# Kernel optimization log

Hardware: AMD Instinct MI355X
Metric: run time of the kernel (lower is better)

The kernel has to match this reference:

```python
import jax, jax.numpy as jnp
import numpy as np

MIN_TIMESCALE = 1.0
MAX_TIMESCALE = 10000.0


def llama_rope(x):
    # x: [B, S, N, H]; LLaMA-style interleaved rotary embedding (pairs along last dim).
    B, S, N, H = x.shape
    half = H // 2
    fraction = 2.0 * jnp.arange(0, half, dtype=jnp.float32) / H
    timescale = MIN_TIMESCALE * (MAX_TIMESCALE / MIN_TIMESCALE) ** fraction  # [half]
    position = jnp.arange(S, dtype=jnp.float32)[None, :, None, None]  # [1,S,1,1]
    sinusoid = position / timescale[None, None, None, :]  # [1,S,1,half]
    sin, cos = jnp.sin(sinusoid), jnp.cos(sinusoid)
    xr = x.astype(jnp.float32).reshape(B, S, N, half, 2)
    x1, x2 = xr[..., 0], xr[..., 1]
    r1 = x1 * cos - x2 * sin
    r2 = x2 * cos + x1 * sin
    out = jnp.stack((r1, r2), axis=-1).reshape(B, S, N, H)
    return out.astype(x.dtype)


def setup_inputs() -> dict:
    key = jax.random.key(0)
    kx, kq, kk, kv, ko = jax.random.split(key, 5)
    B, S, D, N, H = 4, 2048, 2048, 16, 128
    x = jax.random.normal(kx, (B, S, D), dtype=jnp.float32)
    # fan_in-style scaling for projection kernels
    wq = jax.random.normal(kq, (D, N, H), dtype=jnp.float32) / np.sqrt(D)
    wk = jax.random.normal(kk, (D, N, H), dtype=jnp.float32) / np.sqrt(D)
    wv = jax.random.normal(kv, (D, N, H), dtype=jnp.float32) / np.sqrt(D)
    wo = jax.random.normal(ko, (N, H, D), dtype=jnp.float32) / np.sqrt(N * H)
    return {"x": x, "wq": wq, "wk": wk, "wv": wv, "wo": wo}


def reference(x, wq, wk, wv, wo):
    # QKV projections (DenseGeneral with features=(num_heads, head_dim))
    q = jnp.einsum("bsd,dnh->bsnh", x, wq)
    k = jnp.einsum("bsd,dnh->bsnh", x, wk)
    v = jnp.einsum("bsd,dnh->bsnh", x, wv)
    # Fused RoPE on query and key (LLaMA interleaved variant)
    q = llama_rope(q)
    k = llama_rope(k)
    head_dim = q.shape[-1]
    q = q / jnp.sqrt(jnp.asarray(head_dim, q.dtype))
    # Causal flash attention (math equivalent: masked softmax attention)
    S = q.shape[1]
    logits = jnp.einsum("bqnh,bknh->bnqk", q, k)  # [B,N,S,S]
    causal = jnp.tril(jnp.ones((S, S), dtype=bool))
    logits = jnp.where(causal[None, None, :, :], logits, jnp.asarray(-1e30, logits.dtype))
    probs = jax.nn.softmax(logits.astype(jnp.float32), axis=-1).astype(v.dtype)
    attn = jnp.einsum("bnqk,bknh->bqnh", probs, v)  # [B,S,N,H]
    # Output projection (DenseGeneral over axes (-2,-1))
    return jnp.einsum("bqnh,nhd->bqd", attn, wo)
```

## Files before the change

kernel.cpp:

```cpp
#include <hip/hip_runtime.h>
#include <hip/hip_bf16.h>
#include <cmath>

#define S_LEN 2048
#define DDIM  2048
#define NHEAD 16
#define HDIM  128
#define BATCH 4
#define KPAD  152
#define VPAD  40
#define PPAD  40

typedef __bf16 bf16;
typedef __attribute__((ext_vector_type(8))) __bf16 bf16x8;
typedef __attribute__((ext_vector_type(4))) __bf16 bf16x4;
typedef __attribute__((ext_vector_type(4))) float  f32x4;

__device__ __forceinline__ void gl_lds(const bf16* g, bf16* l) {
  __builtin_amdgcn_global_load_lds((const __attribute__((address_space(1))) unsigned*)g,
                                   (__attribute__((address_space(3))) unsigned*)l, 16, 0, 0);
}

__global__ __launch_bounds__(256)
void conv_kernel(const float* __restrict__ x, bf16* __restrict__ y) {
  size_t i = ((size_t)blockIdx.x * 256 + threadIdx.x) * 8;
  float4 a = *(const float4*)&x[i];
  float4 b = *(const float4*)&x[i + 4];
  bf16x8 o;
  o[0] = (bf16)a.x; o[1] = (bf16)a.y; o[2] = (bf16)a.z; o[3] = (bf16)a.w;
  o[4] = (bf16)b.x; o[5] = (bf16)b.y; o[6] = (bf16)b.z; o[7] = (bf16)b.w;
  *(bf16x8*)&y[i] = o;
}

__global__ __launch_bounds__(256)
void twconv_kernel(const float* __restrict__ W, bf16* __restrict__ Wt) {
  __shared__ bf16 tile[64][72];
  const int t  = threadIdx.x;
  const int k0 = blockIdx.x * 64;
  const int n0 = blockIdx.y * 64;
#pragma unroll
  for (int it = 0; it < 4; it++) {
    int k = (t >> 4) + it * 16;
    int n = (t & 15) * 4;
    float4 v = *(const float4*)&W[(size_t)(k0 + k) * DDIM + n0 + n];
    tile[k][n + 0] = (bf16)v.x; tile[k][n + 1] = (bf16)v.y;
    tile[k][n + 2] = (bf16)v.z; tile[k][n + 3] = (bf16)v.w;
  }
  __syncthreads();
#pragma unroll
  for (int it = 0; it < 2; it++) {
    int n  = (t >> 3) + it * 32;
    int kc = (t & 7) * 8;
    bf16x8 o;
#pragma unroll
    for (int j = 0; j < 8; j++) o[j] = tile[kc + j][n];
    *(bf16x8*)&Wt[(size_t)(n0 + n) * DDIM + k0 + kc] = o;
  }
}

template <int MODE>
__global__ __launch_bounds__(512, 2)
void gemm_kernel(const bf16* __restrict__ A, const bf16* __restrict__ Bt,
                 void* __restrict__ Out) {
  __shared__ bf16 As[2][256 * 64];
  __shared__ bf16 Bs[2][256 * 64];

  const int t    = threadIdx.x;
  const int m0   = blockIdx.y * 256;
  const int n0   = blockIdx.x * 256;
  const int lane = t & 63;
  const int wave = t >> 6;
  const int wm   = wave >> 2;
  const int wn   = wave & 3;
  const int quad = lane >> 4;
  const int lm   = lane & 15;
  const int sw   = lm & 7;

  const int lrow   = lane >> 3;
  const int lslot  = lane & 7;
  const int lchunk = lslot ^ lrow;

  const int rA = wm * 128 + wn * 32;
  const int rB = (wn >> 1) * 128 + (wm * 2 + (wn & 1)) * 32;
  const bf16* gA = &A [(size_t)(m0 + rA + lrow) * DDIM + lchunk * 8];
  const bf16* gB = &Bt[(size_t)(n0 + rB + lrow) * DDIM + lchunk * 8];

  f32x4 acc[8][4];
#pragma unroll
  for (int i = 0; i < 8; i++)
#pragma unroll
    for (int j = 0; j < 4; j++) acc[i][j] = (f32x4){0.f, 0.f, 0.f, 0.f};

  auto stage = [&](int k0, int b) {
#pragma unroll
    for (int q = 0; q < 4; q++) {
      gl_lds(gA + (size_t)q * 8 * DDIM + k0, &As[b][(rA + q * 8) * 64]);
      gl_lds(gB + (size_t)q * 8 * DDIM + k0, &Bs[b][(rB + q * 8) * 64]);
    }
  };

  stage(0, 0);
  stage(64, 1);
  asm volatile("s_waitcnt vmcnt(8)" ::: "memory");
  __builtin_amdgcn_s_barrier();

  const int NT = DDIM / 64;
#pragma unroll 2
  for (int tt = 0; tt < NT; ++tt) {
    const bf16* as = &As[tt & 1][0];
    const bf16* bs = &Bs[tt & 1][0];
    bf16x8 af[4], bfr[4];

#pragma unroll
    for (int j = 0; j < 4; j++)
      bfr[j] = *(const bf16x8*)&bs[(wn * 64 + j * 16 + lm) * 64 + 8 * (quad ^ sw)];
#pragma unroll
    for (int i = 0; i < 4; i++)
      af[i] = *(const bf16x8*)&as[(wm * 128 + i * 16 + lm) * 64 + 8 * (quad ^ sw)];
    __builtin_amdgcn_s_setprio(1);
#pragma unroll
    for (int i = 0; i < 4; i++)
#pragma unroll
      for (int j = 0; j < 4; j++)
        acc[i][j] = __builtin_amdgcn_mfma_f32_16x16x32_bf16(af[i], bfr[j], acc[i][j], 0, 0, 0);
    __builtin_amdgcn_s_setprio(0);
    __builtin_amdgcn_sched_barrier(0);

#pragma unroll
    for (int i = 0; i < 4; i++)
      af[i] = *(const bf16x8*)&as[(wm * 128 + 64 + i * 16 + lm) * 64 + 8 * (quad ^ sw)];
    __builtin_amdgcn_s_setprio(1);
#pragma unroll
    for (int i = 0; i < 4; i++)
#pragma unroll
      for (int j = 0; j < 4; j++)
        acc[4 + i][j] = __builtin_amdgcn_mfma_f32_16x16x32_bf16(af[i], bfr[j], acc[4 + i][j], 0, 0, 0);
    __builtin_amdgcn_s_setprio(0);
    __builtin_amdgcn_sched_barrier(0);

#pragma unroll
    for (int j = 0; j < 4; j++)
      bfr[j] = *(const bf16x8*)&bs[(wn * 64 + j * 16 + lm) * 64 + 8 * ((4 + quad) ^ sw)];
#pragma unroll
    for (int i = 0; i < 4; i++)
      af[i] = *(const bf16x8*)&as[(wm * 128 + i * 16 + lm) * 64 + 8 * ((4 + quad) ^ sw)];
    __builtin_amdgcn_s_setprio(1);
#pragma unroll
    for (int i = 0; i < 4; i++)
#pragma unroll
      for (int j = 0; j < 4; j++)
        acc[i][j] = __builtin_amdgcn_mfma_f32_16x16x32_bf16(af[i], bfr[j], acc[i][j], 0, 0, 0);
    __builtin_amdgcn_s_setprio(0);
    __builtin_amdgcn_sched_barrier(0);

#pragma unroll
    for (int i = 0; i < 4; i++)
      af[i] = *(const bf16x8*)&as[(wm * 128 + 64 + i * 16 + lm) * 64 + 8 * ((4 + quad) ^ sw)];
    __builtin_amdgcn_s_setprio(1);
#pragma unroll
    for (int i = 0; i < 4; i++)
#pragma unroll
      for (int j = 0; j < 4; j++)
        acc[4 + i][j] = __builtin_amdgcn_mfma_f32_16x16x32_bf16(af[i], bfr[j], acc[4 + i][j], 0, 0, 0);
    __builtin_amdgcn_s_setprio(0);
    __builtin_amdgcn_sched_barrier(0);

    asm volatile("s_waitcnt lgkmcnt(0)" ::: "memory");
    __builtin_amdgcn_s_barrier();
    if (tt + 2 < NT) {
      stage((tt + 2) * 64, tt & 1);
      asm volatile("s_waitcnt vmcnt(8)" ::: "memory");
      __builtin_amdgcn_s_barrier();
    } else if (tt + 1 < NT) {
      asm volatile("s_waitcnt vmcnt(0)" ::: "memory");
      __builtin_amdgcn_s_barrier();
    }
  }

  const int row_base = m0 + wm * 128;
  const int col_base = n0 + wn * 64;

  if constexpr (MODE == 3) {
    float* O = (float*)Out;
#pragma unroll
    for (int m = 0; m < 8; m++)
#pragma unroll
      for (int j = 0; j < 4; j++)
#pragma unroll
        for (int r = 0; r < 4; r++) {
          int row = row_base + (m >> 2) * 64 + (m & 3) * 16 + quad * 4 + r;
          int col = col_base + j * 16 + lm;
          O[(size_t)row * DDIM + col] = acc[m][j][r];
        }
  } else if constexpr (MODE == 2) {
    bf16* O = (bf16*)Out;
#pragma unroll
    for (int m = 0; m < 8; m++) {
      int row = row_base + (m >> 2) * 64 + (m & 3) * 16 + quad * 4;
      int b = row >> 11, s = row & (S_LEN - 1);
#pragma unroll
      for (int j = 0; j < 4; j++) {
        int col = col_base + j * 16 + lm;
        int head = col >> 7, h = col & (HDIM - 1);
        bf16x4 pk;
#pragma unroll
        for (int r = 0; r < 4; r++) pk[r] = (bf16)acc[m][j][r];
        *(bf16x4*)&O[((size_t)(b * NHEAD + head) * HDIM + h) * S_LEN + s] = pk;
      }
    }
  } else {
    bf16* O = (bf16*)Out;
#pragma unroll
    for (int m = 0; m < 8; m++)
#pragma unroll
      for (int j = 0; j < 4; j++)
#pragma unroll
        for (int r = 0; r < 4; r++) {
          int row = row_base + (m >> 2) * 64 + (m & 3) * 16 + quad * 4 + r;
          int col = col_base + j * 16 + lm;
          int b = row >> 11, s = row & (S_LEN - 1);
          int head = col >> 7, h = col & (HDIM - 1);
          float v = acc[m][j][r];
          float partner = __shfl_xor(v, 1, 64);
          float inv_ts = __expf((float)(h >> 1) * -0.14391156831f);
          float ang = (float)s * inv_ts;
          float sn, cs;
          __sincosf(ang, &sn, &cs);
          float o = ((h & 1) == 0) ? (v * cs - partner * sn) : (v * cs + partner * sn);
          if (MODE == 0) o *= 0.08838834764831845f;
          O[((size_t)(b * NHEAD + head) * S_LEN + s) * HDIM + h] = (bf16)o;
        }
  }
}

__global__ __launch_bounds__(512, 2)
void attn_kernel(const bf16* __restrict__ Q, const bf16* __restrict__ K,
                 const bf16* __restrict__ Vt, bf16* __restrict__ Aout) {
  __shared__ bf16 Ks[2][32 * KPAD];
  __shared__ bf16 Vs[2][128 * VPAD];
  __shared__ bf16 Pl[8][32 * PPAD];
  const int t    = threadIdx.x;
  const int lane = t & 63;
  const int wave = t >> 6;
  const int quad = lane >> 4;
  const int lm   = lane & 15;
  const int lin  = blockIdx.y * 8 + blockIdx.x;
  const int xcd  = lin & 7;
  const int j    = lin >> 3;
  const int bh   = xcd * 8 + (j >> 3);
  const int ja   = j & 7;
  const int a    = (ja & 1) ? (7 - (ja >> 1)) : (ja >> 1);
  const int lobase = a * 128 + wave * 16;
  const int hibase = 2048 - a * 128 - 128 + wave * 16;
  const size_t hb = (size_t)bh * S_LEN * HDIM;
  const bf16* Qh = Q + hb;
  const bf16* Kh = K + hb;
  const bf16* Vh = Vt + hb;
  bf16* P = &Pl[wave][0];

  bf16x8 qflo[4], qfhi[4];
#pragma unroll
  for (int c = 0; c < 4; c++) {
    qflo[c] = *(const bf16x8*)&Qh[(size_t)(lobase + lm) * HDIM + c * 32 + quad * 8];
    qfhi[c] = *(const bf16x8*)&Qh[(size_t)(hibase + lm) * HDIM + c * 32 + quad * 8];
  }

  bf16 onev = (bf16)1.0f;
  bf16x8 ones = {onev, onev, onev, onev, onev, onev, onev, onev};

  f32x4 olo[8], ohi[8];
#pragma unroll
  for (int hc = 0; hc < 8; hc++) {
    olo[hc] = (f32x4){0.f, 0.f, 0.f, 0.f};
    ohi[hc] = (f32x4){0.f, 0.f, 0.f, 0.f};
  }
  f32x4 llo = (f32x4){0.f, 0.f, 0.f, 0.f};
  f32x4 lhi = (f32x4){0.f, 0.f, 0.f, 0.f};

  const int nkt = 64 - 4 * a;
  const int nlo = 4 * a + (wave >> 1) + 1;
  const int nhi = 61 - 4 * a + (wave >> 1);

  const int krow0 = t >> 4, kcol0 = (t & 15) * 8;
  const int vrow0 = t >> 2, vcol0 = (t & 3) * 8;

  bf16x8 kr, vr;

  auto ldk = [&](int kt) {
    kr = *(const bf16x8*)&Kh[(size_t)(kt * 32 + krow0) * HDIM + kcol0];
    vr = *(const bf16x8*)&Vh[(size_t)vrow0 * S_LEN + kt * 32 + vcol0];
  };
  auto stw = [&](int b) {
    *(bf16x8*)&Ks[b][krow0 * KPAD + kcol0] = kr;
    *(bf16x8*)&Vs[b][vrow0 * VPAD + vcol0] = vr;
  };

  ldk(0);
  stw(0);
  if (nkt > 1) ldk(1);
  __syncthreads();

  for (int kt = 0; kt < nkt; kt++) {
    const int kb  = kt * 32;
    const int cur = kt & 1;

    if (kt + 1 < nkt) stw((kt + 1) & 1);
    if (kt + 2 < nkt) ldk(kt + 2);

    const bool hi_act = kt < nhi;
    const bool lo_act = kt < nlo;

    bf16x8 af[2][4];
#pragma unroll
    for (int cb = 0; cb < 2; cb++)
#pragma unroll
      for (int c = 0; c < 4; c++)
        af[cb][c] = *(const bf16x8*)&Ks[cur][(cb * 16 + lm) * KPAD + c * 32 + quad * 8];

    f32x4 shi[2] = {(f32x4){0.f, 0.f, 0.f, 0.f}, (f32x4){0.f, 0.f, 0.f, 0.f}};
    f32x4 slo[2] = {(f32x4){0.f, 0.f, 0.f, 0.f}, (f32x4){0.f, 0.f, 0.f, 0.f}};
    if (hi_act) {
#pragma unroll
      for (int c = 0; c < 4; c++)
#pragma unroll
        for (int cb = 0; cb < 2; cb++)
          shi[cb] = __builtin_amdgcn_mfma_f32_16x16x32_bf16(af[cb][c], qfhi[c], shi[cb], 0, 0, 0);
    }
    if (lo_act) {
#pragma unroll
      for (int c = 0; c < 4; c++)
#pragma unroll
        for (int cb = 0; cb < 2; cb++)
          slo[cb] = __builtin_amdgcn_mfma_f32_16x16x32_bf16(af[cb][c], qflo[c], slo[cb], 0, 0, 0);
    }

    bf16x8 vf[8];
#pragma unroll
    for (int hc = 0; hc < 8; hc++)
      vf[hc] = *(const bf16x8*)&Vs[cur][(hc * 16 + lm) * VPAD + quad * 8];

    if (hi_act) {
#pragma unroll
      for (int cb = 0; cb < 2; cb++) {
        bf16x4 pk;
#pragma unroll
        for (int r = 0; r < 4; r++) {
          int key = kb + cb * 16 + quad * 4 + r;
          float sv = (key <= hibase + lm) ? shi[cb][r] : -3.0e38f;
          pk[r] = (bf16)__expf(sv - 12.0f);
        }
        *(bf16x4*)&P[(16 + lm) * PPAD + cb * 16 + quad * 4] = pk;
      }
    }
    if (lo_act) {
#pragma unroll
      for (int cb = 0; cb < 2; cb++) {
        bf16x4 pk;
#pragma unroll
        for (int r = 0; r < 4; r++) {
          int key = kb + cb * 16 + quad * 4 + r;
          float sv = (key <= lobase + lm) ? slo[cb][r] : -3.0e38f;
          pk[r] = (bf16)__expf(sv - 12.0f);
        }
        *(bf16x4*)&P[lm * PPAD + cb * 16 + quad * 4] = pk;
      }
    }
    __builtin_amdgcn_s_waitcnt(0xC07F);

    if (hi_act) {
      bf16x8 pf = *(const bf16x8*)&P[(16 + lm) * PPAD + quad * 8];
#pragma unroll
      for (int hc = 0; hc < 8; hc++)
        ohi[hc] = __builtin_amdgcn_mfma_f32_16x16x32_bf16(pf, vf[hc], ohi[hc], 0, 0, 0);
      lhi = __builtin_amdgcn_mfma_f32_16x16x32_bf16(pf, ones, lhi, 0, 0, 0);
    }
    if (lo_act) {
      bf16x8 pf = *(const bf16x8*)&P[lm * PPAD + quad * 8];
#pragma unroll
      for (int hc = 0; hc < 8; hc++)
        olo[hc] = __builtin_amdgcn_mfma_f32_16x16x32_bf16(pf, vf[hc], olo[hc], 0, 0, 0);
      llo = __builtin_amdgcn_mfma_f32_16x16x32_bf16(pf, ones, llo, 0, 0, 0);
    }
    __syncthreads();
  }

  const int b = bh >> 4, n = bh & 15;
#pragma unroll
  for (int r = 0; r < 4; r++) {
    float invl = 1.0f / llo[r];
    float invh = 1.0f / lhi[r];
    int ql = lobase + quad * 4 + r;
    int qh = hibase + quad * 4 + r;
    size_t bl = ((size_t)(b * S_LEN + ql) * NHEAD + n) * HDIM;
    size_t bhh = ((size_t)(b * S_LEN + qh) * NHEAD + n) * HDIM;
#pragma unroll
    for (int hc = 0; hc < 8; hc++) {
      Aout[bl  + hc * 16 + lm] = (bf16)(olo[hc][r] * invl);
      Aout[bhh + hc * 16 + lm] = (bf16)(ohi[hc][r] * invh);
    }
  }
}

extern "C" void kernel_launch(void* const* d_in, const int* in_sizes, int n_in,
                              void* d_out, int out_size, void* d_ws, size_t ws_size,
                              hipStream_t stream) {
  const float* x  = (const float*)d_in[0];
  const float* wq = (const float*)d_in[1];
  const float* wk = (const float*)d_in[2];
  const float* wv = (const float*)d_in[3];
  const float* wo = (const float*)d_in[4];
  float* out = (float*)d_out;

  const size_t SZ  = (size_t)BATCH * S_LEN * NHEAD * HDIM;
  const size_t WSZ = (size_t)DDIM * DDIM;
  bf16* Qb = (bf16*)d_ws;
  bf16* Kb = Qb + SZ;
  bf16* Vb = Kb + SZ;
  bf16* Eb = Vb + SZ;

  bf16* WTq = (bf16*)d_out;
  bf16* WTk = WTq + WSZ;
  bf16* WTv = WTk + WSZ;
  bf16* WTo = (bf16*)Qb;

  dim3 blk(256);
  conv_kernel<<<SZ / (256 * 8), blk, 0, stream>>>(x, Eb);
  dim3 gt(32, 32);
  twconv_kernel<<<gt, blk, 0, stream>>>(wq, WTq);
  twconv_kernel<<<gt, blk, 0, stream>>>(wk, WTk);
  twconv_kernel<<<gt, blk, 0, stream>>>(wv, WTv);

  dim3 blk2(512);
  dim3 gg(DDIM / 256, (BATCH * S_LEN) / 256);
  gemm_kernel<0><<<gg, blk2, 0, stream>>>(Eb, WTq, (void*)Qb);
  gemm_kernel<1><<<gg, blk2, 0, stream>>>(Eb, WTk, (void*)Kb);
  gemm_kernel<2><<<gg, blk2, 0, stream>>>(Eb, WTv, (void*)Vb);

  dim3 ga(8, BATCH * NHEAD);
  attn_kernel<<<ga, blk2, 0, stream>>>(Qb, Kb, Vb, Eb);

  twconv_kernel<<<gt, blk, 0, stream>>>(wo, WTo);
  gemm_kernel<3><<<gg, blk2, 0, stream>>>(Eb, WTo, (void*)out);
}
```

Baseline: 574.9 us.

## Use 4-stage K=32 LDS pipeline with interleaved A/B prefetch in GEMM

Restructures the GEMM mainloop from a 2-buffer K=64 pipeline into a 4-slot K=32 ring buffer with prefetch depth 3. The next A and B tiles are issued separately, interleaved between the two MFMA halves, so global-to-LDS traffic overlaps compute more finely. The XOR swizzle on LDS rows is dropped in favour of a plain 32-element row layout. This adds more barriers per unit of K and may bring back LDS bank conflicts.

```diff
diff --git a/kernel.cpp b/kernel.cpp
--- a/kernel.cpp
+++ b/kernel.cpp
@@ -62,8 +62,8 @@
 __global__ __launch_bounds__(512, 2)
 void gemm_kernel(const bf16* __restrict__ A, const bf16* __restrict__ Bt,
                  void* __restrict__ Out) {
-  __shared__ bf16 As[2][256 * 64];
-  __shared__ bf16 Bs[2][256 * 64];
+  __shared__ bf16 As[4][256 * 32];
+  __shared__ bf16 Bs[4][256 * 32];
 
   const int t    = threadIdx.x;
   const int m0   = blockIdx.y * 256;
@@ -74,16 +74,9 @@
   const int wn   = wave & 3;
   const int quad = lane >> 4;
   const int lm   = lane & 15;
-  const int sw   = lm & 7;
-
-  const int lrow   = lane >> 3;
-  const int lslot  = lane & 7;
-  const int lchunk = lslot ^ lrow;
-
-  const int rA = wm * 128 + wn * 32;
-  const int rB = (wn >> 1) * 128 + (wm * 2 + (wn & 1)) * 32;
-  const bf16* gA = &A [(size_t)(m0 + rA + lrow) * DDIM + lchunk * 8];
-  const bf16* gB = &Bt[(size_t)(n0 + rB + lrow) * DDIM + lchunk * 8];
+
+  const int srow   = t >> 2;
+  const int schunk = (t & 3) * 8;
 
   f32x4 acc[8][4];
 #pragma unroll
@@ -91,32 +84,44 @@
 #pragma unroll
     for (int j = 0; j < 4; j++) acc[i][j] = (f32x4){0.f, 0.f, 0.f, 0.f};
 
-  auto stage = [&](int k0, int b) {
-#pragma unroll
-    for (int q = 0; q < 4; q++) {
-      gl_lds(gA + (size_t)q * 8 * DDIM + k0, &As[b][(rA + q * 8) * 64]);
-      gl_lds(gB + (size_t)q * 8 * DDIM + k0, &Bs[b][(rB + q * 8) * 64]);
-    }
+  auto stageA = [&](int T) {
+    const int slot = T & 3;
+    const int k0   = T * 32;
+    gl_lds(&A[(size_t)(m0 + srow) * DDIM + k0 + schunk],       &As[slot][(16 * wave) * 32]);
+    gl_lds(&A[(size_t)(m0 + 128 + srow) * DDIM + k0 + schunk], &As[slot][(128 + 16 * wave) * 32]);
   };
-
-  stage(0, 0);
-  stage(64, 1);
+  auto stageB = [&](int T) {
+    const int slot = T & 3;
+    const int k0   = T * 32;
+    gl_lds(&Bt[(size_t)(n0 + srow) * DDIM + k0 + schunk],       &Bs[slot][(16 * wave) * 32]);
+    gl_lds(&Bt[(size_t)(n0 + 128 + srow) * DDIM + k0 + schunk], &Bs[slot][(128 + 16 * wave) * 32]);
+  };
+
+  stageA(0); stageB(0);
+  stageA(1); stageB(1);
+  stageA(2); stageB(2);
   asm volatile("s_waitcnt vmcnt(8)" ::: "memory");
   __builtin_amdgcn_s_barrier();
 
-  const int NT = DDIM / 64;
-#pragma unroll 2
-  for (int tt = 0; tt < NT; ++tt) {
-    const bf16* as = &As[tt & 1][0];
-    const bf16* bs = &Bs[tt & 1][0];
-    bf16x8 af[4], bfr[4];
+  const int NT = DDIM / 32;
+  bf16x8 bfr[4];
+
+#pragma unroll 1
+  for (int T = 0; T < NT; ++T) {
+    const int slot = T & 3;
+    const bf16* as = &As[slot][0];
+    const bf16* bs = &Bs[slot][0];
+    bf16x8 af[4];
 
 #pragma unroll
     for (int j = 0; j < 4; j++)
-      bfr[j] = *(const bf16x8*)&bs[(wn * 64 + j * 16 + lm) * 64 + 8 * (quad ^ sw)];
+      bfr[j] = *(const bf16x8*)&bs[(wn * 64 + j * 16 + lm) * 32 + quad * 8];
 #pragma unroll
     for (int i = 0; i < 4; i++)
-      af[i] = *(const bf16x8*)&as[(wm * 128 + i * 16 + lm) * 64 + 8 * (quad ^ sw)];
+      af[i] = *(const bf16x8*)&as[(wm * 128 + i * 16 + lm) * 32 + quad * 8];
+    if (T + 3 < NT) stageA(T + 3);
+    __builtin_amdgcn_s_barrier();
+    asm volatile("s_waitcnt lgkmcnt(0)" ::: "memory");
     __builtin_amdgcn_s_setprio(1);
 #pragma unroll
     for (int i = 0; i < 4; i++)
@@ -128,7 +133,10 @@
 
 #pragma unroll
     for (int i = 0; i < 4; i++)
-      af[i] = *(const bf16x8*)&as[(wm * 128 + 64 + i * 16 + lm) * 64 + 8 * (quad ^ sw)];
+      af[i] = *(const bf16x8*)&as[(wm * 128 + 64 + i * 16 + lm) * 32 + quad * 8];
+    if (T + 3 < NT) stageB(T + 3);
+    __builtin_amdgcn_s_barrier();
+    asm volatile("s_waitcnt lgkmcnt(0)" ::: "memory");
     __builtin_amdgcn_s_setprio(1);
 #pragma unroll
     for (int i = 0; i < 4; i++)
@@ -138,43 +146,14 @@
     __builtin_amdgcn_s_setprio(0);
     __builtin_amdgcn_sched_barrier(0);
 
-#pragma unroll
-    for (int j = 0; j < 4; j++)
-      bfr[j] = *(const bf16x8*)&bs[(wn * 64 + j * 16 + lm) * 64 + 8 * ((4 + quad) ^ sw)];
-#pragma unroll
-    for (int i = 0; i < 4; i++)
-      af[i] = *(const bf16x8*)&as[(wm * 128 + i * 16 + lm) * 64 + 8 * ((4 + quad) ^ sw)];
-    __builtin_amdgcn_s_setprio(1);
-#pragma unroll
-    for (int i = 0; i < 4; i++)
-#pragma unroll
-      for (int j = 0; j < 4; j++)
-        acc[i][j] = __builtin_amdgcn_mfma_f32_16x16x32_bf16(af[i], bfr[j], acc[i][j], 0, 0, 0);
-    __builtin_amdgcn_s_setprio(0);
-    __builtin_amdgcn_sched_barrier(0);
-
-#pragma unroll
-    for (int i = 0; i < 4; i++)
-      af[i] = *(const bf16x8*)&as[(wm * 128 + 64 + i * 16 + lm) * 64 + 8 * ((4 + quad) ^ sw)];
-    __builtin_amdgcn_s_setprio(1);
-#pragma unroll
-    for (int i = 0; i < 4; i++)
-#pragma unroll
-      for (int j = 0; j < 4; j++)
-        acc[4 + i][j] = __builtin_amdgcn_mfma_f32_16x16x32_bf16(af[i], bfr[j], acc[4 + i][j], 0, 0, 0);
-    __builtin_amdgcn_s_setprio(0);
-    __builtin_amdgcn_sched_barrier(0);
-
-    asm volatile("s_waitcnt lgkmcnt(0)" ::: "memory");
-    __builtin_amdgcn_s_barrier();
-    if (tt + 2 < NT) {
-      stage((tt + 2) * 64, tt & 1);
+    if (T < NT - 3) {
       asm volatile("s_waitcnt vmcnt(8)" ::: "memory");
-      __builtin_amdgcn_s_barrier();
-    } else if (tt + 1 < NT) {
+    } else if (T == NT - 3) {
+      asm volatile("s_waitcnt vmcnt(4)" ::: "memory");
+    } else if (T == NT - 2) {
       asm volatile("s_waitcnt vmcnt(0)" ::: "memory");
-      __builtin_amdgcn_s_barrier();
-    }
+    }
+    if (T < NT - 1) __builtin_amdgcn_s_barrier();
   }
 
   const int row_base = m0 + wm * 128;
```

Result: no change. 573.8 us (-0.2%).
